# Optimization experiments

Hardware: AMD Instinct MI355X
Metric: run time of the kernel (lower is better)

Reference implementation:

```python
import jax, jax.numpy as jnp
import numpy as np

B = 8192
N_LAYERS = 2
NUM_PATCHES = 196  # 14*14
PATCH_OUT = 4
NUM_CLASSES = 10
IMG = 28


def setup_inputs() -> dict:
    key = jax.random.key(0)
    ks = jax.random.split(key, 5)
    x = jax.random.normal(ks[0], (B, 1, IMG, IMG), dtype=jnp.float32)
    ansatz_params = jax.random.normal(ks[1], (N_LAYERS, 4), dtype=jnp.float32)
    Wc = jax.random.normal(ks[2], (NUM_CLASSES, NUM_PATCHES * PATCH_OUT), dtype=jnp.float32) * 0.02
    bc = jnp.zeros((NUM_CLASSES,), jnp.float32)
    Wr = jax.random.normal(ks[3], (IMG * IMG, NUM_PATCHES * PATCH_OUT), dtype=jnp.float32) * 0.02
    br = jnp.zeros((IMG * IMG,), jnp.float32)
    return {"x": x, "ansatz_params": ansatz_params, "Wc": Wc, "bc": bc, "Wr": Wr, "br": br}


def _ry(state, theta, wire):
    # state: (N,2,2,2,2) real (RY and CNOT are real matrices).
    # RY(t) = [[cos(t/2), -sin(t/2)], [sin(t/2), cos(t/2)]]
    ax = wire + 1
    a0 = jnp.take(state, 0, axis=ax)
    a1 = jnp.take(state, 1, axis=ax)
    h = jnp.asarray(theta) * 0.5
    c, s = jnp.cos(h), jnp.sin(h)
    if c.ndim == 1:  # per-sample angle (N,)
        c = c[:, None, None, None]
        s = s[:, None, None, None]
    return jnp.stack([c * a0 - s * a1, s * a0 + c * a1], axis=ax)


def _cnot(state, ctrl, tgt):
    cax, tax = ctrl + 1, tgt + 1
    s0 = jnp.take(state, 0, axis=cax)
    s1 = jnp.take(state, 1, axis=cax)
    tax2 = tax - 1 if tax > cax else tax  # axis shift after removing ctrl axis
    s1 = jnp.flip(s1, axis=tax2)
    return jnp.stack([s0, s1], axis=cax)


def _simulate(patches_flat, params):
    # patches_flat: (N,4) encode angles; params: (L,4)
    N = patches_flat.shape[0]
    state = jnp.zeros((N, 2, 2, 2, 2), patches_flat.dtype).at[:, 0, 0, 0, 0].set(1.0)
    for w in range(4):
        state = _ry(state, patches_flat[:, w], w)
    for l in range(params.shape[0]):
        for w in range(4):
            state = _ry(state, params[l, w], w)
        for c, t in ((0, 1), (1, 2), (2, 3), (3, 0)):
            state = _cnot(state, c, t)
    p = state * state  # probabilities (real amplitudes)
    feats = jnp.stack(
        [jnp.sum(jnp.take(p, 0, axis=w + 1) - jnp.take(p, 1, axis=w + 1), axis=(1, 2, 3)) for w in range(4)],
        axis=-1,
    )  # (N,4) PauliZ expectations
    return feats


def reference(x, ansatz_params, Wc, bc, Wr, br):
    Bn = x.shape[0]
    # unfold(2,2,2).unfold(3,2,2) -> (B,1,14,14,2,2) -> (B,196,4)
    patches = x.reshape(Bn, 1, 14, 2, 14, 2).transpose(0, 1, 2, 4, 3, 5).reshape(Bn, NUM_PATCHES, 4)
    patches = patches / jnp.max(patches)
    feats = _simulate(patches.reshape(-1, 4), ansatz_params)  # (B*196, 4)
    flat = feats.reshape(Bn, NUM_PATCHES * PATCH_OUT)
    logits = flat @ Wc.T + bc
    recon = (flat @ Wr.T + br).reshape(Bn, 1, IMG, IMG)
    return jax.nn.log_softmax(logits, axis=-1), recon
```

## Files before the change

kernel.cpp:

```cpp
#include <hip/hip_runtime.h>
#include <hip/hip_bf16.h>

#define B_SZ   8192
#define NPATCH 196
#define FEAT   784
#define KP     800
#define IMGPX  784
#define NCLS   10
#define NALL   794
#define NP     896

typedef __attribute__((ext_vector_type(8))) short bf16x8;
typedef __attribute__((ext_vector_type(4))) float fx4;

__device__ inline unsigned f2ord(float f){
    unsigned u = __float_as_uint(f);
    return (u & 0x80000000u) ? ~u : (u | 0x80000000u);
}
__device__ inline float ord2f(unsigned u){
    return (u & 0x80000000u) ? __uint_as_float(u & 0x7FFFFFFFu)
                             : __uint_as_float(~u);
}
__device__ inline unsigned short f2bf(float f){
    union { __hip_bfloat16 h; unsigned short u; } cv;
    cv.h = __float2bfloat16(f);
    return cv.u;
}

__global__ __launch_bounds__(256) void k_maxprep(const float* __restrict__ x,
                                                 const float* __restrict__ Wr,
                                                 const float* __restrict__ Wc,
                                                 const float* __restrict__ ansatz,
                                                 unsigned* __restrict__ maxslot,
                                                 unsigned short* __restrict__ Wall,
                                                 float* __restrict__ trig){
    if (blockIdx.x < 1024){
        const int n4 = (B_SZ * IMGPX) / 4;
        float m = -3.0e38f;
        for (int i = blockIdx.x * 256 + threadIdx.x; i < n4; i += 1024 * 256){
            float4 v = ((const float4*)x)[i];
            m = fmaxf(m, fmaxf(fmaxf(v.x, v.y), fmaxf(v.z, v.w)));
        }
        #pragma unroll
        for (int off = 32; off > 0; off >>= 1)
            m = fmaxf(m, __shfl_down(m, off, 64));
        __shared__ float sm[4];
        int lane = threadIdx.x & 63, wv = threadIdx.x >> 6;
        if (lane == 0) sm[wv] = m;
        __syncthreads();
        if (threadIdx.x == 0){
            m = fmaxf(fmaxf(sm[0], sm[1]), fmaxf(sm[2], sm[3]));
            atomicMax(maxslot, f2ord(m));
        }
        return;
    }
    if (blockIdx.x == 1024 && threadIdx.x < 8){
        float p = ansatz[threadIdx.x];
        trig[threadIdx.x]     = cosf(0.5f * p);
        trig[8 + threadIdx.x] = sinf(0.5f * p);
    }
    int e4  = (blockIdx.x - 1024) * 256 + threadIdx.x;
    int row = e4 / 200;
    int c4  = e4 - row * 200;
    float4 v = {0.f, 0.f, 0.f, 0.f};
    if (c4 < 196){
        int col = c4 * 4;
        if (row < IMGPX)       v = *(const float4*)(Wr + row * FEAT + col);
        else if (row < NALL)   v = *(const float4*)(Wc + (row - IMGPX) * FEAT + col);
    }
    ushort4 o;
    o.x = f2bf(v.x); o.y = f2bf(v.y); o.z = f2bf(v.z); o.w = f2bf(v.w);
    ((ushort4*)Wall)[e4] = o;
}

__global__ __launch_bounds__(256) void k_sim(const float* __restrict__ x,
                                             const unsigned* __restrict__ maxslot,
                                             const float* __restrict__ trig,
                                             unsigned short* __restrict__ flatb){
    int idx = blockIdx.x * 256 + threadIdx.x;
    if (idx >= B_SZ * NPATCH) return;
    int b  = idx / NPATCH;
    int p  = idx - b * NPATCH;
    int pi = p / 14;
    int pj = p - pi * 14;
    const float* base = x + b * IMGPX + pi * 2 * 28 + pj * 2;
    float2 r0 = *(const float2*)(base);
    float2 r1 = *(const float2*)(base + 28);
    float inv = 1.0f / ord2f(*maxslot);
    float th[4] = { r0.x * inv, r0.y * inv, r1.x * inv, r1.y * inv };
    float cw[4], sw[4];
    #pragma unroll
    for (int w = 0; w < 4; ++w) __sincosf(0.5f * th[w], &sw[w], &cw[w]);

    float a[16];
    a[0] = cw[0]; a[8] = sw[0];
    #pragma unroll
    for (int s = 0; s < 16; s += 8){ a[s + 4] = a[s] * sw[1]; a[s] *= cw[1]; }
    #pragma unroll
    for (int s = 0; s < 16; s += 4){ a[s + 2] = a[s] * sw[2]; a[s] *= cw[2]; }
    #pragma unroll
    for (int s = 0; s < 16; s += 2){ a[s + 1] = a[s] * sw[3]; a[s] *= cw[3]; }

    #pragma unroll
    for (int l = 0; l < 2; ++l){
        #pragma unroll
        for (int w = 0; w < 4; ++w){
            float cc = trig[l * 4 + w], ss = trig[8 + l * 4 + w];
            int msk = 8 >> w;
            #pragma unroll
            for (int st = 0; st < 16; ++st){
                if (!(st & msk)){
                    int s1 = st | msk;
                    float a0 = a[st], a1 = a[s1];
                    a[st] = cc * a0 - ss * a1;
                    a[s1] = ss * a0 + cc * a1;
                }
            }
        }
        #pragma unroll
        for (int ci = 0; ci < 4; ++ci){
            int cb = 8 >> ci;
            int tb = 8 >> ((ci + 1) & 3);
            #pragma unroll
            for (int st = 0; st < 16; ++st){
                if ((st & cb) && !(st & tb)){
                    int s1 = st | tb;
                    float tmp = a[st]; a[st] = a[s1]; a[s1] = tmp;
                }
            }
        }
    }
    float f0 = 0, f1 = 0, f2 = 0, f3 = 0;
    #pragma unroll
    for (int st = 0; st < 16; ++st){
        float pp = a[st] * a[st];
        f0 += (st & 8) ? -pp : pp;
        f1 += (st & 4) ? -pp : pp;
        f2 += (st & 2) ? -pp : pp;
        f3 += (st & 1) ? -pp : pp;
    }
    ushort4 o; o.x = f2bf(f0); o.y = f2bf(f1); o.z = f2bf(f2); o.w = f2bf(f3);
    ((ushort4*)(flatb + (size_t)b * KP))[p] = o;
    if (p < 4){
        ushort4 z = {0, 0, 0, 0};
        ((ushort4*)(flatb + (size_t)b * KP + FEAT))[p] = z;
    }
}

__global__ __launch_bounds__(256) void k_gemm(const unsigned short* __restrict__ A,
                                              const unsigned short* __restrict__ Wall,
                                              const float* __restrict__ br,
                                              const float* __restrict__ bc,
                                              float* __restrict__ recon,
                                              float* __restrict__ outls){
    __shared__ unsigned short As[128][32];
    __shared__ unsigned short Bs[128][32];
    __shared__ float sLg[128][NCLS];

    const int t = threadIdx.x;
    const int wv = t >> 6, lane = t & 63;
    const int r = lane & 15, q = lane >> 4;
    const int mb = (wv >> 1) * 64, nb = (wv & 1) * 64;
    const int bm = blockIdx.x, bn = blockIdx.y;

    const unsigned short* gptr[4];
    const unsigned short* lptr[4];
    #pragma unroll
    for (int s = 0; s < 4; ++s){
        int lin = s * 4 + wv;
        int isB = lin >> 3;
        int rb  = (lin & 7) * 16;
        int row = rb + (lane >> 2);
        int kc  = (lane & 3) * 8;
        gptr[s] = (isB ? Wall + (size_t)(bn * 128 + row) * KP
                       : A    + (size_t)(bm * 128 + row) * KP) + kc;
        lptr[s] = isB ? &Bs[rb][0] : &As[rb][0];
    }

    fx4 acc[4][4] = {};

    for (int k0 = 0; k0 < KP; k0 += 32){
        #pragma unroll
        for (int s = 0; s < 4; ++s){
            __builtin_amdgcn_global_load_lds(
                (const __attribute__((address_space(1))) unsigned int*)gptr[s],
                (__attribute__((address_space(3))) unsigned int*)lptr[s],
                16, 0, 0);
            gptr[s] += 32;
        }
        __syncthreads();
        bf16x8 af[4], bf[4];
        #pragma unroll
        for (int i = 0; i < 4; ++i) af[i] = *(const bf16x8*)&As[mb + i * 16 + r][q * 8];
        #pragma unroll
        for (int j = 0; j < 4; ++j) bf[j] = *(const bf16x8*)&Bs[nb + j * 16 + r][q * 8];
        #pragma unroll
        for (int i = 0; i < 4; ++i)
            #pragma unroll
            for (int j = 0; j < 4; ++j)
                acc[i][j] = __builtin_amdgcn_mfma_f32_16x16x32_bf16(af[i], bf[j], acc[i][j], 0, 0, 0);
        __syncthreads();
    }

    #pragma unroll
    for (int i = 0; i < 4; ++i){
        int ml = mb + i * 16 + q * 4;
        int m  = bm * 128 + ml;
        #pragma unroll
        for (int j = 0; j < 4; ++j){
            int n = bn * 128 + nb + j * 16 + r;
            if (n < IMGPX){
                float bias = br[n];
                #pragma unroll
                for (int v = 0; v < 4; ++v)
                    recon[(size_t)(m + v) * IMGPX + n] = acc[i][j][v] + bias;
            } else if (n < NALL){
                float bias = bc[n - IMGPX];
                #pragma unroll
                for (int v = 0; v < 4; ++v)
                    sLg[ml + v][n - IMGPX] = acc[i][j][v] + bias;
            }
        }
    }
    if (bn == 6){
        __syncthreads();
        if (t < 128){
            float v[NCLS];
            float mx = -3.0e38f;
            #pragma unroll
            for (int c = 0; c < NCLS; ++c){ v[c] = sLg[t][c]; mx = fmaxf(mx, v[c]); }
            float s = 0.f;
            #pragma unroll
            for (int c = 0; c < NCLS; ++c) s += expf(v[c] - mx);
            float lse = mx + logf(s);
            size_t rowo = (size_t)(bm * 128 + t) * NCLS;
            #pragma unroll
            for (int c = 0; c < NCLS; ++c) outls[rowo + c] = v[c] - lse;
        }
    }
}

extern "C" void kernel_launch(void* const* d_in, const int* in_sizes, int n_in,
                              void* d_out, int out_size, void* d_ws, size_t ws_size,
                              hipStream_t stream){
    const float* x      = (const float*)d_in[0];
    const float* ansatz = (const float*)d_in[1];
    const float* Wc     = (const float*)d_in[2];
    const float* bc     = (const float*)d_in[3];
    const float* Wr     = (const float*)d_in[4];
    const float* br     = (const float*)d_in[5];
    float* out = (float*)d_out;

    unsigned char* ws = (unsigned char*)d_ws;
    unsigned*       maxslot = (unsigned*)ws;
    float*          trig    = (float*)(ws + 64);
    unsigned short* flatb   = (unsigned short*)(ws + 4096);
    unsigned short* Wall    = (unsigned short*)(ws + 4096 + (size_t)B_SZ * KP * 2);

    hipMemsetAsync(maxslot, 0, 4, stream);
    k_maxprep<<<1724, 256, 0, stream>>>(x, Wr, Wc, ansatz, maxslot, Wall, trig);
    k_sim<<<(B_SZ * NPATCH + 255) / 256, 256, 0, stream>>>(x, maxslot, trig, flatb);
    dim3 g(64, 7);
    k_gemm<<<g, 256, 0, stream>>>(flatb, Wall, br, bc, out + B_SZ * NCLS, out);
}
```

Baseline: 144.0 us.

## Double GEMM K-tile, pack simulator state as float2 pairs, swap grid order

```diff
diff --git a/kernel.cpp b/kernel.cpp
--- a/kernel.cpp
+++ b/kernel.cpp
@@ -4,7 +4,7 @@
 #define B_SZ   8192
 #define NPATCH 196
 #define FEAT   784
-#define KP     800
+#define KP     832
 #define IMGPX  784
 #define NCLS   10
 #define NALL   794
@@ -60,8 +60,9 @@
         trig[8 + threadIdx.x] = sinf(0.5f * p);
     }
     int e4  = (blockIdx.x - 1024) * 256 + threadIdx.x;
-    int row = e4 / 200;
-    int c4  = e4 - row * 200;
+    if (e4 >= NP * (KP / 4)) return;
+    int row = e4 / (KP / 4);
+    int c4  = e4 - row * (KP / 4);
     float4 v = {0.f, 0.f, 0.f, 0.f};
     if (c4 < 196){
         int col = c4 * 4;
@@ -92,56 +93,72 @@
     #pragma unroll
     for (int w = 0; w < 4; ++w) __sincosf(0.5f * th[w], &sw[w], &cw[w]);
 
-    float a[16];
-    a[0] = cw[0]; a[8] = sw[0];
-    #pragma unroll
-    for (int s = 0; s < 16; s += 8){ a[s + 4] = a[s] * sw[1]; a[s] *= cw[1]; }
-    #pragma unroll
-    for (int s = 0; s < 16; s += 4){ a[s + 2] = a[s] * sw[2]; a[s] *= cw[2]; }
-    #pragma unroll
-    for (int s = 0; s < 16; s += 2){ a[s + 1] = a[s] * sw[3]; a[s] *= cw[3]; }
+    float2 s2[8];
+    {
+        float q00 = cw[0] * cw[1], q01 = cw[0] * sw[1];
+        float q10 = sw[0] * cw[1], q11 = sw[0] * sw[1];
+        float pk[8];
+        pk[0] = q00 * cw[2]; pk[1] = q00 * sw[2];
+        pk[2] = q01 * cw[2]; pk[3] = q01 * sw[2];
+        pk[4] = q10 * cw[2]; pk[5] = q10 * sw[2];
+        pk[6] = q11 * cw[2]; pk[7] = q11 * sw[2];
+        #pragma unroll
+        for (int k = 0; k < 8; ++k)
+            s2[k] = make_float2(pk[k] * cw[3], pk[k] * sw[3]);
+    }
 
     #pragma unroll
     for (int l = 0; l < 2; ++l){
         #pragma unroll
-        for (int w = 0; w < 4; ++w){
+        for (int w = 0; w < 3; ++w){
             float cc = trig[l * 4 + w], ss = trig[8 + l * 4 + w];
-            int msk = 8 >> w;
-            #pragma unroll
-            for (int st = 0; st < 16; ++st){
-                if (!(st & msk)){
-                    int s1 = st | msk;
-                    float a0 = a[st], a1 = a[s1];
-                    a[st] = cc * a0 - ss * a1;
-                    a[s1] = ss * a0 + cc * a1;
+            int m = 4 >> w;
+            #pragma unroll
+            for (int k = 0; k < 8; ++k){
+                if (!(k & m)){
+                    float2 a0 = s2[k], a1 = s2[k + m];
+                    s2[k].x     = cc * a0.x - ss * a1.x;
+                    s2[k].y     = cc * a0.y - ss * a1.y;
+                    s2[k + m].x = ss * a0.x + cc * a1.x;
+                    s2[k + m].y = ss * a0.y + cc * a1.y;
                 }
             }
         }
-        #pragma unroll
-        for (int ci = 0; ci < 4; ++ci){
-            int cb = 8 >> ci;
-            int tb = 8 >> ((ci + 1) & 3);
-            #pragma unroll
-            for (int st = 0; st < 16; ++st){
-                if ((st & cb) && !(st & tb)){
-                    int s1 = st | tb;
-                    float tmp = a[st]; a[st] = a[s1]; a[s1] = tmp;
-                }
+        {
+            float cc = trig[l * 4 + 3], ss = trig[8 + l * 4 + 3];
+            #pragma unroll
+            for (int k = 0; k < 8; ++k){
+                float2 v = s2[k];
+                s2[k].x = cc * v.x - ss * v.y;
+                s2[k].y = ss * v.x + cc * v.y;
             }
         }
-    }
-    float f0 = 0, f1 = 0, f2 = 0, f3 = 0;
-    #pragma unroll
-    for (int st = 0; st < 16; ++st){
-        float pp = a[st] * a[st];
-        f0 += (st & 8) ? -pp : pp;
-        f1 += (st & 4) ? -pp : pp;
-        f2 += (st & 2) ? -pp : pp;
-        f3 += (st & 1) ? -pp : pp;
-    }
+        { float2 t = s2[4]; s2[4] = s2[6]; s2[6] = t;
+          t = s2[5]; s2[5] = s2[7]; s2[7] = t; }
+        { float2 t = s2[2]; s2[2] = s2[3]; s2[3] = t;
+          t = s2[6]; s2[6] = s2[7]; s2[7] = t; }
+        #pragma unroll
+        for (int k = 1; k < 8; k += 2) s2[k] = make_float2(s2[k].y, s2[k].x);
+        #pragma unroll
+        for (int k = 0; k < 4; ++k){
+            float t = s2[k].y; s2[k].y = s2[k + 4].y; s2[k + 4].y = t;
+        }
+    }
+
+    float t[8], d[8];
+    #pragma unroll
+    for (int k = 0; k < 8; ++k){
+        float px = s2[k].x * s2[k].x, py = s2[k].y * s2[k].y;
+        t[k] = px + py; d[k] = px - py;
+    }
+    float f0 = (t[0] + t[1] + t[2] + t[3]) - (t[4] + t[5] + t[6] + t[7]);
+    float f1 = (t[0] + t[1] + t[4] + t[5]) - (t[2] + t[3] + t[6] + t[7]);
+    float f2 = (t[0] + t[2] + t[4] + t[6]) - (t[1] + t[3] + t[5] + t[7]);
+    float f3 =  d[0] + d[1] + d[2] + d[3] + d[4] + d[5] + d[6] + d[7];
+
     ushort4 o; o.x = f2bf(f0); o.y = f2bf(f1); o.z = f2bf(f2); o.w = f2bf(f3);
     ((ushort4*)(flatb + (size_t)b * KP))[p] = o;
-    if (p < 4){
+    if (p < 12){
         ushort4 z = {0, 0, 0, 0};
         ((ushort4*)(flatb + (size_t)b * KP + FEAT))[p] = z;
     }
@@ -153,25 +170,25 @@
                                               const float* __restrict__ bc,
                                               float* __restrict__ recon,
                                               float* __restrict__ outls){
-    __shared__ unsigned short As[128][32];
-    __shared__ unsigned short Bs[128][32];
+    __shared__ unsigned short As[128][64];
+    __shared__ unsigned short Bs[128][64];
     __shared__ float sLg[128][NCLS];
 
     const int t = threadIdx.x;
     const int wv = t >> 6, lane = t & 63;
     const int r = lane & 15, q = lane >> 4;
     const int mb = (wv >> 1) * 64, nb = (wv & 1) * 64;
-    const int bm = blockIdx.x, bn = blockIdx.y;
-
-    const unsigned short* gptr[4];
-    const unsigned short* lptr[4];
-    #pragma unroll
-    for (int s = 0; s < 4; ++s){
+    const int bn = blockIdx.x, bm = blockIdx.y;
+
+    const unsigned short* gptr[8];
+    const unsigned short* lptr[8];
+    #pragma unroll
+    for (int s = 0; s < 8; ++s){
         int lin = s * 4 + wv;
-        int isB = lin >> 3;
-        int rb  = (lin & 7) * 16;
-        int row = rb + (lane >> 2);
-        int kc  = (lane & 3) * 8;
+        int isB = lin >> 4;
+        int rb  = (lin & 15) * 8;
+        int row = rb + (lane >> 3);
+        int kc  = (lane & 7) * 8;
         gptr[s] = (isB ? Wall + (size_t)(bn * 128 + row) * KP
                        : A    + (size_t)(bm * 128 + row) * KP) + kc;
         lptr[s] = isB ? &Bs[rb][0] : &As[rb][0];
@@ -179,26 +196,34 @@
 
     fx4 acc[4][4] = {};
 
-    for (int k0 = 0; k0 < KP; k0 += 32){
-        #pragma unroll
-        for (int s = 0; s < 4; ++s){
+    for (int k0 = 0; k0 < KP; k0 += 64){
+        #pragma unroll
+        for (int s = 0; s < 8; ++s){
             __builtin_amdgcn_global_load_lds(
                 (const __attribute__((address_space(1))) unsigned int*)gptr[s],
                 (__attribute__((address_space(3))) unsigned int*)lptr[s],
                 16, 0, 0);
-            gptr[s] += 32;
-        }
-        __syncthreads();
-        bf16x8 af[4], bf[4];
-        #pragma unroll
-        for (int i = 0; i < 4; ++i) af[i] = *(const bf16x8*)&As[mb + i * 16 + r][q * 8];
-        #pragma unroll
-        for (int j = 0; j < 4; ++j) bf[j] = *(const bf16x8*)&Bs[nb + j * 16 + r][q * 8];
+            gptr[s] += 64;
+        }
+        __syncthreads();
+        bf16x8 af[4][2], bf[4][2];
         #pragma unroll
         for (int i = 0; i < 4; ++i)
             #pragma unroll
-            for (int j = 0; j < 4; ++j)
-                acc[i][j] = __builtin_amdgcn_mfma_f32_16x16x32_bf16(af[i], bf[j], acc[i][j], 0, 0, 0);
+            for (int h = 0; h < 2; ++h)
+                af[i][h] = *(const bf16x8*)&As[mb + i * 16 + r][h * 32 + q * 8];
+        #pragma unroll
+        for (int j = 0; j < 4; ++j)
+            #pragma unroll
+            for (int h = 0; h < 2; ++h)
+                bf[j][h] = *(const bf16x8*)&Bs[nb + j * 16 + r][h * 32 + q * 8];
+        #pragma unroll
+        for (int h = 0; h < 2; ++h)
+            #pragma unroll
+            for (int i = 0; i < 4; ++i)
+                #pragma unroll
+                for (int j = 0; j < 4; ++j)
+                    acc[i][j] = __builtin_amdgcn_mfma_f32_16x16x32_bf16(af[i][h], bf[j][h], acc[i][j], 0, 0, 0);
         __syncthreads();
     }
 
@@ -258,8 +283,8 @@
     unsigned short* Wall    = (unsigned short*)(ws + 4096 + (size_t)B_SZ * KP * 2);
 
     hipMemsetAsync(maxslot, 0, 4, stream);
-    k_maxprep<<<1724, 256, 0, stream>>>(x, Wr, Wc, ansatz, maxslot, Wall, trig);
+    k_maxprep<<<1752, 256, 0, stream>>>(x, Wr, Wc, ansatz, maxslot, Wall, trig);
     k_sim<<<(B_SZ * NPATCH + 255) / 256, 256, 0, stream>>>(x, maxslot, trig, flatb);
-    dim3 g(64, 7);
+    dim3 g(7, 64);
     k_gemm<<<g, 256, 0, stream>>>(flatb, Wall, br, bc, out + B_SZ * NCLS, out);
 }
```

After: 137.6 us. -4.5%, faster.
